# Performance work log

Hardware: AMD Instinct MI355X
Metric: run time of the kernel (lower is better)

Reference implementation:

```python
import jax, jax.numpy as jnp
import numpy as np
import math

E = 100
V = 3
DK = 100
B = 8192
S = 100
T = 10


def setup_inputs() -> dict:
    key = jax.random.key(0)
    ks = jax.random.split(key, 11)
    bound = 1.0 / math.sqrt(E)  # nn.Linear default init range
    def lin(k):
        k1, k2 = jax.random.split(k)
        w = jax.random.uniform(k1, (E, E), jnp.float32, -bound, bound)
        b = jax.random.uniform(k2, (E,), jnp.float32, -bound, bound)
        return w, b
    fc1_w, fc1_b = lin(ks[0])
    fc2_w, fc2_b = lin(ks[1])
    fc3_w, fc3_b = lin(ks[2])
    fc4_w, fc4_b = lin(ks[3])
    vk = jax.random.uniform(ks[4], (V, E), jnp.float32)  # torch.rand
    x = jax.random.normal(ks[5], (B, S, E), jnp.float32)
    tag_embedding = jax.random.normal(ks[6], (B, T, E), jnp.float32)
    return {
        "x": x, "tag_embedding": tag_embedding, "vk": vk,
        "fc1_w": fc1_w, "fc1_b": fc1_b, "fc2_w": fc2_w, "fc2_b": fc2_b,
        "fc3_w": fc3_w, "fc3_b": fc3_b, "fc4_w": fc4_w, "fc4_b": fc4_b,
    }


def reference(x, tag_embedding, vk, fc1_w, fc1_b, fc2_w, fc2_b, fc3_w, fc3_b, fc4_w, fc4_b):
    scale = 1.0 / math.sqrt(DK)
    pad = jnp.float32(-(2.0 ** 32) + 1.0)

    # Stage 1: user behaviors attend over virtual kernels
    of1 = x @ fc1_w.T + fc1_b                      # [B,S,E]
    of2 = vk @ fc2_w.T + fc2_b                     # [V,E]
    m1 = jnp.einsum('bse,ve->bsv', of1, of2) * scale  # [B,S,V]
    sign = jnp.sign(jnp.sum(jnp.abs(x), axis=2))[:, :, None]  # [B,S,1]
    m1 = jnp.where(sign == 0, pad, m1)             # mask zero-padded behaviors
    sm1 = jax.nn.softmax(m1, axis=1)               # softmax over S (dim=1, as in torch)
    ws1 = jnp.einsum('bsv,bse->bve', sm1, of1)     # [B,V,E]

    # Stage 2: tag attends over virtual-kernel summaries
    of3 = vk @ fc3_w.T + fc3_b                     # [V,E]
    of4 = tag_embedding @ fc4_w.T + fc4_b          # [B,T,E]
    m2 = jnp.einsum('bte,ve->btv', of4, of3) * scale  # [B,T,V]
    sm2 = jax.nn.softmax(m2, axis=1)               # softmax over T (dim=1, as in torch)
    user_emb = jnp.einsum('btv,bve->bte', sm2, ws1)  # [B,T,E]

    return jnp.sum(user_emb * tag_embedding, axis=2)  # [B,T]
```

## Files before the change

### kernel.cpp

```cpp
#include <hip/hip_runtime.h>
#include <math.h>

#define E 100
#define V 3
#define S 100
#define T 10
#define NB 8192
#define SCALE 0.1f
#define PADV  (-4294967295.0f)

#define WS_H  0
#define WS_G  304
#define WS_B1 608
#define WS_C1 708
#define WS_C2 712


__global__ __launch_bounds__(256) void prep_kernel(const float* __restrict__ vk,
        const float* __restrict__ fc1w, const float* __restrict__ fc1b,
        const float* __restrict__ fc2w, const float* __restrict__ fc2b,
        const float* __restrict__ fc3w, const float* __restrict__ fc3b,
        const float* __restrict__ fc4w, const float* __restrict__ fc4b,
        float* __restrict__ ws)
{
    __shared__ __align__(16) float wsm[E * E];
    __shared__ __align__(16) float ofs[V * E];
    const int t   = threadIdx.x;
    const int blk = blockIdx.x;
    const float* WA = blk ? fc4w : fc1w;
    const float* WB = blk ? fc3w : fc2w;
    const float* bB = blk ? fc3b : fc2b;
    const float* bA = blk ? fc4b : fc1b;

    for (int i = t; i < E * E / 4; i += 256)
        *(float4*)(&wsm[4 * i]) = *(const float4*)(WA + 4 * i);

    for (int o = t; o < V * E; o += 256) {
        int v = o / E, e = o % E;
        const float* vr = vk + v * E;
        const float* wr = WB + e * E;
        float acc = bB[e];
        for (int k = 0; k < E; k += 4) {
            float4 a = *(const float4*)(vr + k);
            float4 w = *(const float4*)(wr + k);
            acc += a.x * w.x + a.y * w.y + a.z * w.z + a.w * w.w;
        }
        ofs[o] = acc;
    }
    __syncthreads();

    for (int o = t; o < V * E; o += 256) {
        int v = o / E, k = o % E;
        float acc = 0.f;
        for (int e = 0; e < E; ++e) acc += ofs[v * E + e] * wsm[e * E + k];
        ws[(blk ? WS_G : WS_H) + o] = acc * SCALE;
    }
    if (t < V) {
        float acc = 0.f;
        for (int e = 0; e < E; ++e) acc += bA[e] * ofs[t * E + e];
        ws[(blk ? WS_C2 : WS_C1) + t] = acc * SCALE;
    }
    if (blk == 0 && t < E) ws[WS_B1 + t] = fc1b[t];
}

__global__ __launch_bounds__(256, 8) void mvke_main(const float* __restrict__ x,
        const float* __restrict__ tag, const float* __restrict__ fc1w,
        const float* __restrict__ ws, float* __restrict__ out)
{
    __shared__ __align__(16) float tg[T * E];
    __shared__ __align__(16) float Hs[V * E];
    __shared__ __align__(16) float Gs[V * E];
    __shared__ __align__(16) float b1s[E];
    __shared__ float cs[8];
    __shared__ __align__(16) float m1s[V * S];
    __shared__ __align__(16) float sm1s[V * S];
    __shared__ __align__(16) float ys[V * E];
    __shared__ __align__(16) float ws1s[V * E];
    __shared__ float m2s[T * V];
    __shared__ float sm2s[T * V];
    __shared__ float p3[32];

    const int t = threadIdx.x;
    const int b = blockIdx.x;
    const float* xb = x   + (size_t)b * (S * E);
    const float* tb = tag + (size_t)b * (T * E);

    for (int i = t; i < T * E / 4; i += 256)
        *(float4*)(&tg[4 * i]) = *(const float4*)(tb + 4 * i);
    if (t < 75)        *(float4*)(&Hs[4 * t])          = *(const float4*)(ws + WS_H  + 4 * t);
    else if (t < 150)  *(float4*)(&Gs[4 * (t - 75)])   = *(const float4*)(ws + WS_G  + 4 * (t - 75));
    else if (t < 175)  *(float4*)(&b1s[4 * (t - 150)]) = *(const float4*)(ws + WS_B1 + 4 * (t - 150));
    else if (t < 183)  cs[t - 175] = ws[WS_C1 + (t - 175)];
    __syncthreads();

    if (t < S) {
        const float* xr = xb + t * E;
        float a0 = cs[0], a1 = cs[1], a2 = cs[2], ra = 0.f;
        #pragma unroll 5
        for (int k = 0; k < E; k += 4) {
            float4 xv = *(const float4*)(xr + k);
            float4 h0 = *(const float4*)(&Hs[k]);
            float4 h1 = *(const float4*)(&Hs[E + k]);
            float4 h2 = *(const float4*)(&Hs[2 * E + k]);
            a0 += xv.x * h0.x + xv.y * h0.y + xv.z * h0.z + xv.w * h0.w;
            a1 += xv.x * h1.x + xv.y * h1.y + xv.z * h1.z + xv.w * h1.w;
            a2 += xv.x * h2.x + xv.y * h2.y + xv.z * h2.z + xv.w * h2.w;
            ra += fabsf(xv.x) + fabsf(xv.y) + fabsf(xv.z) + fabsf(xv.w);
        }
        bool z = (ra == 0.f);
        m1s[t]         = z ? PADV : a0;
        m1s[S + t]     = z ? PADV : a1;
        m1s[2 * S + t] = z ? PADV : a2;
    } else if (t >= 128 && t < 128 + T * V) {
        int o = t - 128, tt = o / V, v = o % V;
        const float* tr = &tg[tt * E];
        const float* gr = &Gs[v * E];
        float acc = cs[4 + v];
        #pragma unroll 5
        for (int k = 0; k < E; k += 4) {
            float4 a = *(const float4*)(tr + k);
            float4 g = *(const float4*)(gr + k);
            acc += a.x * g.x + a.y * g.y + a.z * g.z + a.w * g.w;
        }
        m2s[o] = acc;
    }
    __syncthreads();

    {
        int wv = t >> 6, lane = t & 63;
        if (wv < V) {
            float x1 = m1s[wv * S + lane];
            float x2 = (lane + 64 < S) ? m1s[wv * S + lane + 64] : -INFINITY;
            float mx = fmaxf(x1, x2);
            for (int d = 32; d > 0; d >>= 1) mx = fmaxf(mx, __shfl_xor(mx, d));
            float e1 = __expf(x1 - mx);
            float e2 = (lane + 64 < S) ? __expf(x2 - mx) : 0.f;
            float sm = e1 + e2;
            for (int d = 32; d > 0; d >>= 1) sm += __shfl_xor(sm, d);
            float inv = 1.f / sm;
            sm1s[wv * S + lane] = e1 * inv;
            if (lane + 64 < S) sm1s[wv * S + lane + 64] = e2 * inv;
        } else if (lane < V) {
            float mm[T];
            float mx = -INFINITY;
            for (int tt = 0; tt < T; ++tt) { mm[tt] = m2s[tt * V + lane]; mx = fmaxf(mx, mm[tt]); }
            float ee[T];
            float sum = 0.f;
            for (int tt = 0; tt < T; ++tt) { ee[tt] = __expf(mm[tt] - mx); sum += ee[tt]; }
            float inv = 1.f / sum;
            for (int tt = 0; tt < T; ++tt) sm2s[tt * V + lane] = ee[tt] * inv;
        }
    }
    __syncthreads();

    for (int o = t; o < V * E; o += 256) {
        int v = o / E, k = o % E;
        const float* smr = &sm1s[v * S];
        const float* xc  = xb + k;
        float a0 = 0.f, a1 = 0.f;
        #pragma unroll 4
        for (int s = 0; s < S; s += 2) {
            a0 += smr[s]     * xc[s * E];
            a1 += smr[s + 1] * xc[(s + 1) * E];
        }
        ys[o] = a0 + a1;
    }
    __syncthreads();

    for (int o = t; o < V * E; o += 256) {
        int v = o / E, e = o % E;
        const float* wr = fc1w + e * E;
        const float* yr = &ys[v * E];
        float acc = b1s[e];
        #pragma unroll 5
        for (int k = 0; k < E; k += 4) {
            float4 w  = *(const float4*)(wr + k);
            float4 yv = *(const float4*)(&yr[k]);
            acc += w.x * yv.x + w.y * yv.y + w.z * yv.z + w.w * yv.w;
        }
        ws1s[o] = acc;
    }
    __syncthreads();

    if (t < T * V) {
        int tt = t / V, v = t % V;
        const float* wr = &ws1s[v * E];
        const float* tr = &tg[tt * E];
        float acc = 0.f;
        #pragma unroll 5
        for (int k = 0; k < E; k += 4) {
            float4 w = *(const float4*)(wr + k);
            float4 a = *(const float4*)(tr + k);
            acc += w.x * a.x + w.y * a.y + w.z * a.z + w.w * a.w;
        }
        p3[t] = sm2s[t] * acc;
    }
    __syncthreads();
    if (t < T)
        out[(size_t)b * T + t] = p3[t * V] + p3[t * V + 1] + p3[t * V + 2];
}

extern "C" void kernel_launch(void* const* d_in, const int* in_sizes, int n_in,
                              void* d_out, int out_size, void* d_ws, size_t ws_size,
                              hipStream_t stream) {
    const float* x    = (const float*)d_in[0];
    const float* tag  = (const float*)d_in[1];
    const float* vk   = (const float*)d_in[2];
    const float* fc1w = (const float*)d_in[3];
    const float* fc1b = (const float*)d_in[4];
    const float* fc2w = (const float*)d_in[5];
    const float* fc2b = (const float*)d_in[6];
    const float* fc3w = (const float*)d_in[7];
    const float* fc3b = (const float*)d_in[8];
    const float* fc4w = (const float*)d_in[9];
    const float* fc4b = (const float*)d_in[10];
    float* out = (float*)d_out;
    float* ws  = (float*)d_ws;

    hipLaunchKernelGGL(prep_kernel, dim3(2), dim3(256), 0, stream,
                       vk, fc1w, fc1b, fc2w, fc2b, fc3w, fc3b, fc4w, fc4b, ws);
    hipLaunchKernelGGL(mvke_main, dim3(NB), dim3(256), 0, stream,
                       x, tag, fc1w, ws, out);
}
```

Baseline: 664.8 us.

## Stage x tile into LDS via async global_load_lds and read it for weighted sum

Each block now issues asynchronous global-to-LDS loads of its full 40KB x tile (and tag tile) at kernel start, overlapping them with the score computation, and the later softmax-weighted reduction over S reads x from LDS instead of re-reading global memory with strided accesses. The tag dot products read tag from global directly since the LDS copy may not have arrived yet. The inner reduction is unrolled to four accumulators. The added 40KB of LDS lowers occupancy (launch bound changed from 8 to 3 blocks), trading latency hiding for removing the second pass over x from global/L2.

```diff
diff --git a/kernel.cpp b/kernel.cpp
--- a/kernel.cpp
+++ b/kernel.cpp
@@ -14,6 +14,16 @@
 #define WS_B1 608
 #define WS_C1 708
 #define WS_C2 712
+
+#define GLOAD_LDS16(g, l) __builtin_amdgcn_global_load_lds( \
+    (const __attribute__((address_space(1))) void*)(g),      \
+    (__attribute__((address_space(3))) void*)(l), 16, 0, 0)
+
+#define LGKM_BARRIER() do {                                   \
+    asm volatile("s_waitcnt lgkmcnt(0)" ::: "memory");        \
+    __builtin_amdgcn_s_barrier();                             \
+    __builtin_amdgcn_sched_barrier(0);                        \
+} while (0)
 
 
 __global__ __launch_bounds__(256) void prep_kernel(const float* __restrict__ vk,
@@ -63,10 +73,11 @@
     if (blk == 0 && t < E) ws[WS_B1 + t] = fc1b[t];
 }
 
-__global__ __launch_bounds__(256, 8) void mvke_main(const float* __restrict__ x,
+__global__ __launch_bounds__(256, 3) void mvke_main(const float* __restrict__ x,
         const float* __restrict__ tag, const float* __restrict__ fc1w,
         const float* __restrict__ ws, float* __restrict__ out)
 {
+    __shared__ __align__(16) float xs[S * E];
     __shared__ __align__(16) float tg[T * E];
     __shared__ __align__(16) float Hs[V * E];
     __shared__ __align__(16) float Gs[V * E];
@@ -85,13 +96,23 @@
     const float* xb = x   + (size_t)b * (S * E);
     const float* tb = tag + (size_t)b * (T * E);
 
-    for (int i = t; i < T * E / 4; i += 256)
-        *(float4*)(&tg[4 * i]) = *(const float4*)(tb + 4 * i);
+    #pragma unroll
+    for (int j = 0; j < 9; ++j) {
+        int i = t + 256 * j;
+        GLOAD_LDS16(xb + 4 * i, &xs[4 * i]);
+    }
+    if (t < 196) {
+        int i = t + 2304;
+        GLOAD_LDS16(xb + 4 * i, &xs[4 * i]);
+    }
+    if (t < 250)
+        GLOAD_LDS16(tb + 4 * t, &tg[4 * t]);
+
     if (t < 75)        *(float4*)(&Hs[4 * t])          = *(const float4*)(ws + WS_H  + 4 * t);
     else if (t < 150)  *(float4*)(&Gs[4 * (t - 75)])   = *(const float4*)(ws + WS_G  + 4 * (t - 75));
     else if (t < 175)  *(float4*)(&b1s[4 * (t - 150)]) = *(const float4*)(ws + WS_B1 + 4 * (t - 150));
     else if (t < 183)  cs[t - 175] = ws[WS_C1 + (t - 175)];
-    __syncthreads();
+    LGKM_BARRIER();
 
     if (t < S) {
         const float* xr = xb + t * E;
@@ -113,7 +134,7 @@
         m1s[2 * S + t] = z ? PADV : a2;
     } else if (t >= 128 && t < 128 + T * V) {
         int o = t - 128, tt = o / V, v = o % V;
-        const float* tr = &tg[tt * E];
+        const float* tr = tb + tt * E;
         const float* gr = &Gs[v * E];
         float acc = cs[4 + v];
         #pragma unroll 5
@@ -124,7 +145,7 @@
         }
         m2s[o] = acc;
     }
-    __syncthreads();
+    LGKM_BARRIER();
 
     {
         int wv = t >> 6, lane = t & 63;
@@ -151,19 +172,25 @@
             for (int tt = 0; tt < T; ++tt) sm2s[tt * V + lane] = ee[tt] * inv;
         }
     }
-    __syncthreads();
+    LGKM_BARRIER();
+
+    asm volatile("s_waitcnt vmcnt(0)" ::: "memory");
+    __builtin_amdgcn_s_barrier();
+    __builtin_amdgcn_sched_barrier(0);
 
     for (int o = t; o < V * E; o += 256) {
         int v = o / E, k = o % E;
         const float* smr = &sm1s[v * S];
-        const float* xc  = xb + k;
-        float a0 = 0.f, a1 = 0.f;
-        #pragma unroll 4
-        for (int s = 0; s < S; s += 2) {
+        const float* xc  = &xs[k];
+        float a0 = 0.f, a1 = 0.f, a2 = 0.f, a3 = 0.f;
+        #pragma unroll 5
+        for (int s = 0; s < S; s += 4) {
             a0 += smr[s]     * xc[s * E];
             a1 += smr[s + 1] * xc[(s + 1) * E];
-        }
-        ys[o] = a0 + a1;
+            a2 += smr[s + 2] * xc[(s + 2) * E];
+            a3 += smr[s + 3] * xc[(s + 3) * E];
+        }
+        ys[o] = (a0 + a1) + (a2 + a3);
     }
     __syncthreads();
 
```

Result: faster. 558.6 us (-16.0%).
